# Performance work log

Measured on AMD Instinct MI355X. Metric: run time of the kernel, lower is better.

The kernel has to match this reference:

```python
import jax, jax.numpy as jnp
import numpy as np

B, L, E = 256, 8192, 64
PS_HIGH, PS_LOW = 3, 12
THR = 1.5
WINDOW = 9
K = 5
MAXP = (L + PS_HIGH - 1) // PS_HIGH  # max possible patches per row


def setup_inputs() -> dict:
    key = jax.random.key(0)
    k1, k2, k3, k4, k5 = jax.random.split(key, 5)
    x = jax.random.randint(k1, (B, L), 0, K)  # int tokens in [0, K)
    w1 = jax.random.normal(k2, (E, 1), jnp.float32)        # Linear(1, E) weight
    b1 = jax.random.normal(k3, (E,), jnp.float32) * 0.1
    w2 = jax.random.normal(k4, (E, E), jnp.float32) / np.float32(np.sqrt(E))  # Linear(E, E) weight
    b2 = jax.random.normal(k5, (E,), jnp.float32) * 0.1
    return {"x": x, "w1": w1, "b1": b1, "w2": w2, "b2": b2}


def calc_entropy(x):
    # one-hot counts in a sliding window of size WINDOW (same as conv1d with ones kernel, groups=K)
    oh = jax.nn.one_hot(jnp.clip(x, 0, K - 1), K, dtype=jnp.float32)  # [B, L, K]
    oh = jnp.moveaxis(oh, -1, 1)                                       # [B, K, L]
    pad = WINDOW // 2
    padded = jnp.pad(oh, ((0, 0), (0, 0), (pad, pad)))                 # [B, K, L+2*pad]
    cs = jnp.cumsum(padded, axis=-1)
    csz = jnp.pad(cs, ((0, 0), (0, 0), (1, 0)))
    counts = csz[..., WINDOW:] - csz[..., :-WINDOW]                    # [B, K, L]
    total = jnp.clip(counts.sum(axis=1, keepdims=True), 1e-12, None)
    probs = counts / total
    entropy = -(probs * jnp.log2(probs + 1e-12)).sum(axis=1)           # [B, L]
    return entropy


def seg_row(cs_row, ent_row):
    # cs_row: [L+1] prefix sums of x (float); ent_row: [L] entropy
    def step(i, _):
        ent_i = ent_row[jnp.minimum(i, L - 1)]
        psize = jnp.where(ent_i > THR, PS_HIGH, PS_LOW).astype(jnp.int32)
        j = jnp.minimum(i + psize, L)
        valid = i < L
        mean = (cs_row[j] - cs_row[i]) / jnp.maximum(j - i, 1).astype(jnp.float32)
        return j, (mean, valid)

    _, (means, valids) = jax.lax.scan(step, jnp.int32(0), None, length=MAXP)
    return means, valids  # [MAXP], [MAXP]


def reference(x, w1, b1, w2, b2):
    entropy = calc_entropy(x)
    # prefix sums for O(1) per-patch means
    cs = jnp.pad(jnp.cumsum(x.astype(jnp.float32), axis=1), ((0, 0), (1, 0)))  # [B, L+1]
    means, valids = jax.vmap(seg_row)(cs, entropy)  # [B, MAXP], [B, MAXP]
    # batched tiny MLP over all candidate patches: Linear(1,E) -> ReLU -> Linear(E,E)
    h = jax.nn.relu(means[..., None] * w1[:, 0] + b1)  # [B, MAXP, E]
    vec = h @ w2.T + b2                                # [B, MAXP, E]
    m = valids[..., None].astype(jnp.float32)
    blt_features = (vec * m).sum(axis=1) / m.sum(axis=1)  # [B, E]
    return blt_features, entropy
```

## Files before the change

### kernel.cpp

```cpp
#include <hip/hip_runtime.h>


constexpr int B_ = 256;
constexpr int L_ = 8192;
constexpr int E_ = 64;
constexpr int CHUNK = 128;
constexpr int NCH = L_ / CHUNK;
constexpr int MAXPC = 44;

__global__ __launch_bounds__(256, 1)
void entropy_patcher_kernel(const int* __restrict__ x,
                            const float* __restrict__ w1,
                            const float* __restrict__ b1,
                            const float* __restrict__ w2,
                            const float* __restrict__ b2,
                            float* __restrict__ dout) {
  __shared__ __align__(16) unsigned int codesPad[L_ + 8];
  __shared__ __align__(16) unsigned char tok8[L_];
  __shared__ unsigned long long maskS[L_ / 64];
  __shared__ __align__(16) float meanbuf[NCH][MAXPC];
  __shared__ unsigned char exitT[NCH][12];
  __shared__ unsigned char offC[NCH];
  __shared__ int cntC[NCH];
  __shared__ int waveTot[4];
  __shared__ float Sred[4][E_];
  __shared__ float partG[4][E_];
  __shared__ float avgv[E_];
  __shared__ float rcpTab[16];
  __shared__ int Pcount;

  const int tid  = threadIdx.x;
  const int lane = tid & 63;
  const int wv   = tid >> 6;
  const int b    = blockIdx.x;

  const int* xr = x + b * L_;
  float* entOut = dout + (size_t)B_ * E_ + (size_t)b * L_;

  if (tid < 16) rcpTab[tid] = 1.0f / (float)(tid < 1 ? 1 : tid);
  if (tid < 4) { codesPad[tid] = 0u; codesPad[4 + L_ + tid] = 0u; }
  #pragma unroll
  for (int k = 0; k < 8; ++k) {
    int g = tid + 256 * k;
    int4 v = ((const int4*)xr)[g];
    unsigned t0 = (unsigned)v.x, t1 = (unsigned)v.y;
    unsigned t2 = (unsigned)v.z, t3 = (unsigned)v.w;
    ((unsigned*)tok8)[g] = t0 | (t1 << 8) | (t2 << 16) | (t3 << 24);
    unsigned c0 = t0 > 4u ? 4u : t0, c1 = t1 > 4u ? 4u : t1;
    unsigned c2 = t2 > 4u ? 4u : t2, c3 = t3 > 4u ? 4u : t3;
    uint4 cv;
    cv.x = 1u << (6 * c0); cv.y = 1u << (6 * c1);
    cv.z = 1u << (6 * c2); cv.w = 1u << (6 * c3);
    ((uint4*)(codesPad + 4))[g] = cv;
  }
  __syncthreads();

  for (int k = 0; k < 32; ++k) {
    int p = tid + 256 * k;
    unsigned s = 0;
    #pragma unroll
    for (int j = 0; j < 9; ++j) s += codesPad[p + j];
    float rT = 1.0f / 9.0f;
    if (p < 4 || p > L_ - 5) {
      int lo = p - 4; if (lo < 0) lo = 0;
      int hi = p + 4; if (hi > L_ - 1) hi = L_ - 1;
      rT = 1.0f / (float)(hi - lo + 1);
    }
    float ent = 0.0f;
    #pragma unroll
    for (int cc = 0; cc < 5; ++cc) {
      float pr = (float)((s >> (6 * cc)) & 63u) * rT;
      ent -= pr * __log2f(pr + 1e-12f);
    }
    entOut[p] = ent;
    unsigned long long bal = __ballot(ent > 1.5f);
    if (lane == 0) maskS[(unsigned)p >> 6] = bal;
  }
  __syncthreads();

  {
    uint4 a0 = ((const uint4*)tok8)[2 * tid];
    uint4 a1 = ((const uint4*)tok8)[2 * tid + 1];
    unsigned wd[8] = {a0.x, a0.y, a0.z, a0.w, a1.x, a1.y, a1.z, a1.w};
    int tv[32];
    int localSum = 0;
    #pragma unroll
    for (int j = 0; j < 32; ++j) {
      tv[j] = (int)((wd[j >> 2] >> (8 * (j & 3))) & 0xffu);
      localSum += tv[j];
    }
    int v = localSum;
    #pragma unroll
    for (int d = 1; d < 64; d <<= 1) {
      int t = __shfl_up(v, d, 64);
      if (lane >= d) v += t;
    }
    if (lane == 63) waveTot[wv] = v;
    __syncthreads();
    int base = 0;
    for (int q = 0; q < wv; ++q) base += waveTot[q];
    float* cs = (float*)codesPad;
    float acc = (float)(base + v - localSum);
    float4* csv = (float4*)cs;
    #pragma unroll
    for (int j4 = 0; j4 < 8; ++j4) {
      float4 f;
      f.x = acc; acc += (float)tv[4 * j4 + 0];
      f.y = acc; acc += (float)tv[4 * j4 + 1];
      f.z = acc; acc += (float)tv[4 * j4 + 2];
      f.w = acc; acc += (float)tv[4 * j4 + 3];
      csv[8 * tid + j4] = f;
    }
    if (tid == 255) cs[L_] = acc;
  }
  __syncthreads();

  #pragma unroll
  for (int jj = 0; jj < 3; ++jj) {
    int c = lane;
    int o = wv + 4 * jj;
    int p = c * CHUNK + o;
    int end = c * CHUNK + CHUNK;
    while (p < end) {
      int bit = (int)((maskS[p >> 6] >> (p & 63)) & 1ULL);
      p += bit ? 3 : 12;
    }
    exitT[c][o] = (unsigned char)(p - end);
  }
  __syncthreads();
  if (tid == 0) {
    unsigned char o = 0;
    for (int c = 0; c < NCH; ++c) { offC[c] = o; o = exitT[c][o]; }
  }
  __syncthreads();

  if (tid < NCH) {
    const float* cs = (const float*)codesPad;
    int c = tid;
    int p = c * CHUNK + (int)offC[c];
    int end = c * CHUNK + CHUNK;
    int n = 0;
    while (p < end) {
      int bit = (int)((maskS[p >> 6] >> (p & 63)) & 1ULL);
      int ps = bit ? 3 : 12;
      int j = p + ps; if (j > L_) j = L_;
      float num = cs[j] - cs[p];
      meanbuf[c][n++] = num * rcpTab[j - p];
      p += ps;
    }
    cntC[c] = n;
  }
  __syncthreads();

  if (tid == 0) {
    int P = 0;
    #pragma unroll
    for (int c = 0; c < NCH; ++c) P += cntC[c];
    Pcount = P;
  }
  {
    float w1v = w1[lane];
    float b1v = b1[lane];
    float S = 0.0f;
    for (int c = wv; c < NCH; c += 4) {
      int n = cntC[c];
      const float* mb = &meanbuf[c][0];
      int j = 0;
      for (; j + 4 <= n; j += 4) {
        float4 m4 = *((const float4*)(mb + j));
        S += fmaxf(fmaf(m4.x, w1v, b1v), 0.0f);
        S += fmaxf(fmaf(m4.y, w1v, b1v), 0.0f);
        S += fmaxf(fmaf(m4.z, w1v, b1v), 0.0f);
        S += fmaxf(fmaf(m4.w, w1v, b1v), 0.0f);
      }
      for (; j < n; ++j)
        S += fmaxf(fmaf(mb[j], w1v, b1v), 0.0f);
    }
    Sred[wv][lane] = S;
  }
  __syncthreads();

  if (tid < E_) {
    float s = Sred[0][tid] + Sred[1][tid] + Sred[2][tid] + Sred[3][tid];
    avgv[tid] = s / (float)Pcount;
  }
  __syncthreads();
  {
    int e = lane, q = wv;
    float acc = 0.0f;
    #pragma unroll
    for (int kk = 0; kk < 16; ++kk) {
      int k = 16 * q + kk;
      acc = fmaf(avgv[k], w2[e * 64 + k], acc);
    }
    partG[q][e] = acc;
  }
  __syncthreads();
  if (tid < E_) {
    float r = partG[0][tid] + partG[1][tid] + partG[2][tid] + partG[3][tid] + b2[tid];
    dout[(size_t)b * E_ + tid] = r;
  }
}

extern "C" void kernel_launch(void* const* d_in, const int* in_sizes, int n_in,
                              void* d_out, int out_size, void* d_ws, size_t ws_size,
                              hipStream_t stream) {
  const int*   x  = (const int*)d_in[0];
  const float* w1 = (const float*)d_in[1];
  const float* b1 = (const float*)d_in[2];
  const float* w2 = (const float*)d_in[3];
  const float* b2 = (const float*)d_in[4];
  float* out = (float*)d_out;
  entropy_patcher_kernel<<<B_, 256, 0, stream>>>(x, w1, b1, w2, b2, out);
}
```

Measured before the change: 99.82 us.

## Rewrite patcher kernel with 1024 threads, sliding-window entropy and parallel chunk-offset scan

Moves from 256 to 1024 threads per block, each handling 8 consecutive tokens. Entropy is computed with a register sliding window and a precomputed pair-entropy lookup table instead of per-position log2 calls. The serial single-thread chain of chunk offsets is replaced by a wave-level parallel composition of exit-offset tables. Several shared buffers and barriers are removed. In exchange it adds a 4-bit table-composition scan whose cost is uncertain, and higher per-thread register pressure.

After: 82.68 us. -17.2%, faster.

```diff
diff --git a/kernel.cpp b/kernel.cpp
--- a/kernel.cpp
+++ b/kernel.cpp
@@ -1,33 +1,36 @@
 #include <hip/hip_runtime.h>
+#include <math.h>
 
 
 constexpr int B_ = 256;
 constexpr int L_ = 8192;
 constexpr int E_ = 64;
+constexpr int T_ = 1024;
+constexpr int PT = 8;
 constexpr int CHUNK = 128;
 constexpr int NCH = L_ / CHUNK;
 constexpr int MAXPC = 44;
 
-__global__ __launch_bounds__(256, 1)
+__global__ __launch_bounds__(1024)
 void entropy_patcher_kernel(const int* __restrict__ x,
                             const float* __restrict__ w1,
                             const float* __restrict__ b1,
                             const float* __restrict__ w2,
                             const float* __restrict__ b2,
                             float* __restrict__ dout) {
-  __shared__ __align__(16) unsigned int codesPad[L_ + 8];
-  __shared__ __align__(16) unsigned char tok8[L_];
-  __shared__ unsigned long long maskS[L_ / 64];
+  __shared__ __align__(16) unsigned char tok8p[8 + L_ + 8];
+  __shared__ __align__(16) float csBuf[L_ + 4];
   __shared__ __align__(16) float meanbuf[NCH][MAXPC];
+  __shared__ __align__(16) float pairTab[100];
+  __shared__ __align__(16) unsigned char maskBytes[T_];
   __shared__ unsigned char exitT[NCH][12];
-  __shared__ unsigned char offC[NCH];
+  __shared__ float rcpTab[13];
   __shared__ int cntC[NCH];
-  __shared__ int waveTot[4];
-  __shared__ float Sred[4][E_];
-  __shared__ float partG[4][E_];
+  __shared__ int waveTot[16];
+  __shared__ float Sred[16][E_];
+  __shared__ float partG[16][E_];
   __shared__ float avgv[E_];
-  __shared__ float rcpTab[16];
-  __shared__ int Pcount;
+  __shared__ int PcountS;
 
   const int tid  = threadIdx.x;
   const int lane = tid & 63;
@@ -37,132 +40,174 @@
   const int* xr = x + b * L_;
   float* entOut = dout + (size_t)B_ * E_ + (size_t)b * L_;
 
-  if (tid < 16) rcpTab[tid] = 1.0f / (float)(tid < 1 ? 1 : tid);
-  if (tid < 4) { codesPad[tid] = 0u; codesPad[4 + L_ + tid] = 0u; }
-  #pragma unroll
-  for (int k = 0; k < 8; ++k) {
-    int g = tid + 256 * k;
-    int4 v = ((const int4*)xr)[g];
-    unsigned t0 = (unsigned)v.x, t1 = (unsigned)v.y;
-    unsigned t2 = (unsigned)v.z, t3 = (unsigned)v.w;
-    ((unsigned*)tok8)[g] = t0 | (t1 << 8) | (t2 << 16) | (t3 << 24);
-    unsigned c0 = t0 > 4u ? 4u : t0, c1 = t1 > 4u ? 4u : t1;
-    unsigned c2 = t2 > 4u ? 4u : t2, c3 = t3 > 4u ? 4u : t3;
-    uint4 cv;
-    cv.x = 1u << (6 * c0); cv.y = 1u << (6 * c1);
-    cv.z = 1u << (6 * c2); cv.w = 1u << (6 * c3);
-    ((uint4*)(codesPad + 4))[g] = cv;
-  }
-  __syncthreads();
-
-  for (int k = 0; k < 32; ++k) {
-    int p = tid + 256 * k;
-    unsigned s = 0;
-    #pragma unroll
-    for (int j = 0; j < 9; ++j) s += codesPad[p + j];
-    float rT = 1.0f / 9.0f;
-    if (p < 4 || p > L_ - 5) {
-      int lo = p - 4; if (lo < 0) lo = 0;
-      int hi = p + 4; if (hi > L_ - 1) hi = L_ - 1;
-      rT = 1.0f / (float)(hi - lo + 1);
-    }
-    float ent = 0.0f;
-    #pragma unroll
-    for (int cc = 0; cc < 5; ++cc) {
-      float pr = (float)((s >> (6 * cc)) & 63u) * rT;
-      ent -= pr * __log2f(pr + 1e-12f);
-    }
-    entOut[p] = ent;
-    unsigned long long bal = __ballot(ent > 1.5f);
-    if (lane == 0) maskS[(unsigned)p >> 6] = bal;
-  }
-  __syncthreads();
-
+  const int4 v0 = ((const int4*)xr)[2 * tid];
+  const int4 v1 = ((const int4*)xr)[2 * tid + 1];
+  unsigned pw0 = (unsigned)v0.x | ((unsigned)v0.y << 8) |
+                 ((unsigned)v0.z << 16) | ((unsigned)v0.w << 24);
+  unsigned pw1 = (unsigned)v1.x | ((unsigned)v1.y << 8) |
+                 ((unsigned)v1.z << 16) | ((unsigned)v1.w << 24);
+  *(uint2*)(tok8p + 8 + 8 * tid) = make_uint2(pw0, pw1);
+  if (tid == 0) *(uint2*)(tok8p) = make_uint2(~0u, ~0u);
+  if (tid == 1) *(uint2*)(tok8p + 8 + L_) = make_uint2(~0u, ~0u);
+  if (tid < 100) {
+    int a = tid / 10, c = tid - 10 * a;
+    float pa = (float)a / 9.0f, pb = (float)c / 9.0f;
+    float fa = -(pa * log2f(pa + 1e-12f));
+    float fb = -(pb * log2f(pb + 1e-12f));
+    pairTab[tid] = fa + fb;
+  }
+  if (tid >= 100 && tid < 113) {
+    int n = tid - 100;
+    rcpTab[n] = 1.0f / (float)(n == 0 ? 1 : n);
+  }
+  __syncthreads();
+
+  unsigned long long tw0 = *(const unsigned long long*)(tok8p + 8 * tid);
+  unsigned long long tw1 = *(const unsigned long long*)(tok8p + 8 * tid + 8);
+  unsigned long long tw2 = *(const unsigned long long*)(tok8p + 8 * tid + 16);
+  unsigned code[20];
+  #pragma unroll
+  for (int l = 4; l < 20; ++l) {
+    unsigned byte = (l < 8)  ? (unsigned)((tw0 >> (8 * l)) & 0xff)
+                  : (l < 16) ? (unsigned)((tw1 >> (8 * (l - 8))) & 0xff)
+                             : (unsigned)((tw2 >> (8 * (l - 16))) & 0xff);
+    code[l] = (byte <= 4u) ? (1u << (6 * byte)) : 0u;
+  }
+  unsigned s = 0;
+  #pragma unroll
+  for (int l = 4; l <= 12; ++l) s += code[l];
+  float entv[PT];
+  #pragma unroll
+  for (int q = 0; q < PT; ++q) {
+    if (q) s += code[q + 12] - code[q + 3];
+    unsigned a  = s & 63u,        bb = (s >> 6) & 63u, cc = (s >> 12) & 63u;
+    unsigned dd = (s >> 18) & 63u, ee = (s >> 24) & 63u;
+    entv[q] = pairTab[a * 10u + bb] + pairTab[cc * 10u + dd] + pairTab[ee * 10u];
+  }
+  if (tid == 0 || tid == T_ - 1) {
+    #pragma unroll
+    for (int q = 0; q < PT; ++q) {
+      int p = 8 * tid + q;
+      if (p < 4 || p >= L_ - 4) {
+        unsigned ss = 0;
+        for (int l = q + 4; l <= q + 12; ++l) ss += code[l];
+        unsigned cn[5] = { ss & 63u, (ss >> 6) & 63u, (ss >> 12) & 63u,
+                           (ss >> 18) & 63u, (ss >> 24) & 63u };
+        float rT = 1.0f / (float)(cn[0] + cn[1] + cn[2] + cn[3] + cn[4]);
+        float ent = 0.f;
+        for (int k2 = 0; k2 < 5; ++k2) {
+          float pr = (float)cn[k2] * rT;
+          ent -= pr * log2f(pr + 1e-12f);
+        }
+        entv[q] = ent;
+      }
+    }
+  }
+  ((float4*)entOut)[2 * tid]     = make_float4(entv[0], entv[1], entv[2], entv[3]);
+  ((float4*)entOut)[2 * tid + 1] = make_float4(entv[4], entv[5], entv[6], entv[7]);
+  unsigned mbyte = 0;
+  #pragma unroll
+  for (int q = 0; q < PT; ++q) mbyte |= (entv[q] > 1.5f ? 1u : 0u) << q;
+  maskBytes[tid] = (unsigned char)mbyte;
+
+  int tk[8];
+  #pragma unroll
+  for (int j = 0; j < 4; ++j) {
+    tk[j]     = (int)((pw0 >> (8 * j)) & 0xffu);
+    tk[4 + j] = (int)((pw1 >> (8 * j)) & 0xffu);
+  }
+  int ls = tk[0] + tk[1] + tk[2] + tk[3] + tk[4] + tk[5] + tk[6] + tk[7];
+  int incl = ls;
+  #pragma unroll
+  for (int d = 1; d < 64; d <<= 1) {
+    int up = __shfl_up(incl, d, 64);
+    if (lane >= d) incl += up;
+  }
+  if (lane == 63) waveTot[wv] = incl;
+  __syncthreads();
+  int base = 0;
+  #pragma unroll
+  for (int q = 0; q < 16; ++q) base += (q < wv) ? waveTot[q] : 0;
+  float acc = (float)(base + incl - ls);
   {
-    uint4 a0 = ((const uint4*)tok8)[2 * tid];
-    uint4 a1 = ((const uint4*)tok8)[2 * tid + 1];
-    unsigned wd[8] = {a0.x, a0.y, a0.z, a0.w, a1.x, a1.y, a1.z, a1.w};
-    int tv[32];
-    int localSum = 0;
-    #pragma unroll
-    for (int j = 0; j < 32; ++j) {
-      tv[j] = (int)((wd[j >> 2] >> (8 * (j & 3))) & 0xffu);
-      localSum += tv[j];
-    }
-    int v = localSum;
+    float4 c0, c1;
+    c0.x = acc; acc += (float)tk[0]; c0.y = acc; acc += (float)tk[1];
+    c0.z = acc; acc += (float)tk[2]; c0.w = acc; acc += (float)tk[3];
+    c1.x = acc; acc += (float)tk[4]; c1.y = acc; acc += (float)tk[5];
+    c1.z = acc; acc += (float)tk[6]; c1.w = acc; acc += (float)tk[7];
+    ((float4*)csBuf)[2 * tid] = c0; ((float4*)csBuf)[2 * tid + 1] = c1;
+    if (tid == T_ - 1) csBuf[L_] = acc;
+  }
+
+  unsigned long long m0 = 0, m1 = 0;
+  if (tid < 768) {
+    int c = tid & 63, o = tid >> 6;
+    m0 = *(const unsigned long long*)(maskBytes + 16 * c);
+    m1 = *(const unsigned long long*)(maskBytes + 16 * c + 8);
+    int p = o;
+    while (p < CHUNK) {
+      unsigned long long mm = (p & 64) ? m1 : m0;
+      p += ((mm >> (p & 63)) & 1ULL) ? 3 : 12;
+    }
+    exitT[c][o] = (unsigned char)(p - CHUNK);
+  }
+  __syncthreads();
+
+  int myOff = 0;
+  if (tid < 64) {
+    const unsigned* ep = (const unsigned*)&exitT[tid][0];
+    unsigned u0 = ep[0], u1 = ep[1], u2 = ep[2];
+    auto nib = [](unsigned w) {
+      return (w & 0xFu) | ((w >> 4) & 0xF0u) | ((w >> 8) & 0xF00u) | ((w >> 12) & 0xF000u);
+    };
+    unsigned long long tab = (unsigned long long)nib(u0)
+                           | ((unsigned long long)nib(u1) << 16)
+                           | ((unsigned long long)nib(u2) << 32);
     #pragma unroll
     for (int d = 1; d < 64; d <<= 1) {
-      int t = __shfl_up(v, d, 64);
-      if (lane >= d) v += t;
-    }
-    if (lane == 63) waveTot[wv] = v;
-    __syncthreads();
-    int base = 0;
-    for (int q = 0; q < wv; ++q) base += waveTot[q];
-    float* cs = (float*)codesPad;
-    float acc = (float)(base + v - localSum);
-    float4* csv = (float4*)cs;
-    #pragma unroll
-    for (int j4 = 0; j4 < 8; ++j4) {
-      float4 f;
-      f.x = acc; acc += (float)tv[4 * j4 + 0];
-      f.y = acc; acc += (float)tv[4 * j4 + 1];
-      f.z = acc; acc += (float)tv[4 * j4 + 2];
-      f.w = acc; acc += (float)tv[4 * j4 + 3];
-      csv[8 * tid + j4] = f;
-    }
-    if (tid == 255) cs[L_] = acc;
-  }
-  __syncthreads();
-
-  #pragma unroll
-  for (int jj = 0; jj < 3; ++jj) {
-    int c = lane;
-    int o = wv + 4 * jj;
-    int p = c * CHUNK + o;
-    int end = c * CHUNK + CHUNK;
-    while (p < end) {
-      int bit = (int)((maskS[p >> 6] >> (p & 63)) & 1ULL);
-      p += bit ? 3 : 12;
-    }
-    exitT[c][o] = (unsigned char)(p - end);
-  }
-  __syncthreads();
-  if (tid == 0) {
-    unsigned char o = 0;
-    for (int c = 0; c < NCH; ++c) { offC[c] = o; o = exitT[c][o]; }
-  }
-  __syncthreads();
-
-  if (tid < NCH) {
-    const float* cs = (const float*)codesPad;
+      unsigned long long other =
+          (unsigned long long)__shfl_up((long long)tab, d, 64);
+      if (lane >= d) {
+        unsigned long long nt = 0;
+        #pragma unroll
+        for (int e = 0; e < 12; ++e) {
+          unsigned oe  = (unsigned)((other >> (4 * e)) & 15ULL);
+          unsigned val = (unsigned)((tab >> (4 * oe)) & 15ULL);
+          nt |= (unsigned long long)val << (4 * e);
+        }
+        tab = nt;
+      }
+    }
+    unsigned long long prev = (unsigned long long)__shfl_up((long long)tab, 1, 64);
+    myOff = (lane == 0) ? 0 : (int)(prev & 15ULL);
+
     int c = tid;
-    int p = c * CHUNK + (int)offC[c];
-    int end = c * CHUNK + CHUNK;
+    int p = CHUNK * c + myOff;
+    const int end = CHUNK * c + CHUNK;
+    float csp = csBuf[p];
     int n = 0;
     while (p < end) {
-      int bit = (int)((maskS[p >> 6] >> (p & 63)) & 1ULL);
-      int ps = bit ? 3 : 12;
+      int lp = p - CHUNK * c;
+      unsigned long long mm = (lp & 64) ? m1 : m0;
+      int ps = ((mm >> (lp & 63)) & 1ULL) ? 3 : 12;
       int j = p + ps; if (j > L_) j = L_;
-      float num = cs[j] - cs[p];
-      meanbuf[c][n++] = num * rcpTab[j - p];
-      p += ps;
+      float csj = csBuf[j];
+      meanbuf[c][n++] = (csj - csp) * rcpTab[j - p];
+      csp = csj; p = j;
     }
     cntC[c] = n;
-  }
-  __syncthreads();
-
-  if (tid == 0) {
-    int P = 0;
-    #pragma unroll
-    for (int c = 0; c < NCH; ++c) P += cntC[c];
-    Pcount = P;
-  }
+    int tot = n;
+    #pragma unroll
+    for (int d2 = 32; d2; d2 >>= 1) tot += __shfl_xor(tot, d2, 64);
+    if (lane == 0) PcountS = tot;
+  }
+  __syncthreads();
+
   {
-    float w1v = w1[lane];
-    float b1v = b1[lane];
+    const float w1v = w1[lane];
+    const float b1v = b1[lane];
     float S = 0.0f;
-    for (int c = wv; c < NCH; c += 4) {
+    for (int c = wv; c < NCH; c += 16) {
       int n = cntC[c];
       const float* mb = &meanbuf[c][0];
       int j = 0;
@@ -173,31 +218,33 @@
         S += fmaxf(fmaf(m4.z, w1v, b1v), 0.0f);
         S += fmaxf(fmaf(m4.w, w1v, b1v), 0.0f);
       }
-      for (; j < n; ++j)
-        S += fmaxf(fmaf(mb[j], w1v, b1v), 0.0f);
+      for (; j < n; ++j) S += fmaxf(fmaf(mb[j], w1v, b1v), 0.0f);
     }
     Sred[wv][lane] = S;
   }
   __syncthreads();
-
-  if (tid < E_) {
-    float s = Sred[0][tid] + Sred[1][tid] + Sred[2][tid] + Sred[3][tid];
-    avgv[tid] = s / (float)Pcount;
-  }
-  __syncthreads();
+  if (tid < 64) {
+    float sm = 0.f;
+    #pragma unroll
+    for (int q = 0; q < 16; ++q) sm += Sred[q][tid];
+    avgv[tid] = sm / (float)PcountS;
+  }
+  __syncthreads();
+
   {
-    int e = lane, q = wv;
-    float acc = 0.0f;
-    #pragma unroll
-    for (int kk = 0; kk < 16; ++kk) {
-      int k = 16 * q + kk;
-      acc = fmaf(avgv[k], w2[e * 64 + k], acc);
-    }
-    partG[q][e] = acc;
-  }
-  __syncthreads();
-  if (tid < E_) {
-    float r = partG[0][tid] + partG[1][tid] + partG[2][tid] + partG[3][tid] + b2[tid];
+    float acc2 = 0.f;
+    #pragma unroll
+    for (int kk = 0; kk < 4; ++kk) {
+      int k = 4 * wv + kk;
+      acc2 = fmaf(avgv[k], w2[lane * 64 + k], acc2);
+    }
+    partG[wv][lane] = acc2;
+  }
+  __syncthreads();
+  if (tid < 64) {
+    float r = b2[tid];
+    #pragma unroll
+    for (int q = 0; q < 16; ++q) r += partG[q][tid];
     dout[(size_t)b * E_ + tid] = r;
   }
 }
@@ -211,5 +258,5 @@
   const float* w2 = (const float*)d_in[3];
   const float* b2 = (const float*)d_in[4];
   float* out = (float*)d_out;
-  entropy_patcher_kernel<<<B_, 256, 0, stream>>>(x, w1, b1, w2, b2, out);
+  entropy_patcher_kernel<<<B_, T_, 0, stream>>>(x, w1, b1, w2, b2, out);
 }
```
